# Performance work log

Hardware: AMD Instinct MI355X
Metric: run time of the kernel (lower is better)

Reference implementation:

```python
import jax, jax.numpy as jnp
import numpy as np

B, N, F, D, TOPK, EXTRA = 32, 128, 10, 64, 20, 25
BN = B * N
EPS = 1e-5
SLOPE = 0.2  # GDN GraphLayer leaky_relu negative slope


def _cosine(a, b):
    na = jnp.maximum(jnp.linalg.norm(a, axis=-1), 1e-12)
    nb = jnp.maximum(jnp.linalg.norm(b, axis=-1), 1e-12)
    return (a @ b.T) / (na[:, None] * nb[None, :])


def _segment_softmax(logits, seg, num):
    m = jax.ops.segment_max(logits, seg, num_segments=num)
    m = jnp.where(jnp.isfinite(m), m, 0.0)  # empty segments
    e = jnp.exp(logits - m[seg])
    s = jax.ops.segment_sum(e, seg, num_segments=num)
    return e / jnp.maximum(s[seg], 1e-12)


def setup_inputs() -> dict:
    key = jax.random.key(0)
    ks = jax.random.split(key, 12)
    r = lambda i, shape, s=1.0: jax.random.normal(ks[i], shape, dtype=jnp.float32) * s
    return dict(
        data=r(0, (B, N, F)),
        emb=r(1, (N, D)) * 0.3,                       # nn.Embedding(node_num, dim)
        W1=r(2, (F, D)) * (1.0 / np.sqrt(F)),         # GraphLayer lin
        att_i1=r(3, (2 * D,)) * 0.1,                  # att on concat(h, emb)
        att_j1=r(4, (2 * D,)) * 0.1,
        bias1=jnp.zeros((D,), jnp.float32),
        bn1_g=jnp.ones((D,), jnp.float32),
        bn1_b=jnp.zeros((D,), jnp.float32),
        P=r(5, (BN, BN)) * (1.0 / np.sqrt(BN)),       # extra_pram
        W2=r(6, (D, D)) * (1.0 / np.sqrt(D)),         # GraphLayer1 lin
        att_i2=r(7, (D,)) * 0.1,
        att_j2=r(8, (D,)) * 0.1,
        bias2=jnp.zeros((D,), jnp.float32),
        bnO_g=jnp.ones((D,), jnp.float32),
        bnO_b=jnp.zeros((D,), jnp.float32),
        W_out=r(9, (D, 1)) * (1.0 / np.sqrt(D)),      # OutLayer Linear(dim,1)
        b_out=jnp.zeros((1,), jnp.float32),
        org_edge_index=jnp.zeros((2, 2), jnp.int32),  # dead arg in original forward
    )


def _forward(data, emb, W1, att_i1, att_j1, bias1, bn1_g, bn1_b, P, W2,
             att_i2, att_j2, bias2, bnO_g, bnO_b, W_out, b_out):
    x = data.reshape(BN, F)

    # ---- learned top-k graph from detached embedding cosine similarity ----
    w = jax.lax.stop_gradient(emb)              # weights_arr = detach()
    cos = _cosine(w, w)                         # [N, N]
    topv, topi = jax.lax.top_k(cos, TOPK)       # [N, TOPK]
    cos_w = jnp.tile(topv.reshape(-1), B)       # [B*N*TOPK]
    src0 = topi.reshape(-1)                     # gated_j (source)
    dst0 = jnp.repeat(jnp.arange(N), TOPK)      # gated_i (target)
    offs = jnp.repeat(jnp.arange(B) * N, N * TOPK)
    src = jnp.tile(src0, B) + offs
    dst = jnp.tile(dst0, B) + offs

    # ---- GraphLayer (GAT-style with embedding keys, edge weight = cos) ----
    all_emb = jnp.tile(emb, (B, 1))             # [BN, D]
    h = x @ W1                                  # [BN, D]
    kf = jnp.concatenate([h, all_emb], axis=-1) # [BN, 2D]
    si, sj = kf @ att_i1, kf @ att_j1           # [BN]
    score = jax.nn.leaky_relu(si[dst] + sj[src], SLOPE) * cos_w
    alpha = _segment_softmax(score, dst, BN)
    agg = jax.ops.segment_sum(h[src] * alpha[:, None], dst, num_segments=BN) + bias1
    mu, var = agg.mean(0), agg.var(0)           # BatchNorm1d (batch stats)
    gcn = jax.nn.relu(bn1_g * (agg - mu) / jnp.sqrt(var + EPS) + bn1_b)

    # ---- extra-feature branch (always taken: P is [BN, BN]) ----
    ef = P.T @ gcn                              # (gcn_out.T @ P).T
    g = jnp.concatenate([gcn, ef], axis=0)      # [2BN, D]
    cos2 = _cosine(g, g)                        # [2BN, 2BN]
    topv2, topi2 = jax.lax.top_k(cos2, EXTRA)
    corrs = topv2[:BN].reshape(-1)              # [BN*EXTRA]
    src2 = jnp.repeat(jnp.arange(BN), EXTRA)    # extra_i = edge_index[0] (source)
    dst2 = topi2[:BN].reshape(-1)               # extra_j = edge_index[1] (target)

    # ---- GraphLayer1 (no embedding keys, no BN in GNNLayer1.forward) ----
    h2 = g @ W2                                 # [2BN, D]
    s2 = jax.nn.leaky_relu((h2 @ att_i2)[dst2] + (h2 @ att_j2)[src2], SLOPE) * corrs
    alpha2 = _segment_softmax(s2, dst2, 2 * BN)
    agg2 = jax.ops.segment_sum(h2[src2] * alpha2[:, None], dst2, num_segments=2 * BN) + bias2
    gcn2 = jax.nn.relu(agg2)[:BN]

    # ---- output head: mul by embedding, BN over channels, Linear(D,1) ----
    x3 = gcn2.reshape(B, N, D) * emb[None]      # [B, N, D]
    mu2, var2 = x3.mean((0, 1)), x3.var((0, 1)) # BatchNorm1d over channel D
    x4 = jax.nn.relu(bnO_g * (x3 - mu2) / jnp.sqrt(var2 + EPS) + bnO_b)
    out = x4 @ W_out + b_out                    # [B, N, 1]; dropout = identity (eval)
    return out.reshape(-1, N)                   # [B, N]


def reference(data, emb, W1, att_i1, att_j1, bias1, bn1_g, bn1_b, P, W2,
              att_i2, att_j2, bias2, bnO_g, bnO_b, W_out, b_out, org_edge_index):
    # org_edge_index is dead in the original forward (only cached, never consumed)
    return _forward(data, emb, W1, att_i1, att_j1, bias1, bn1_g, bn1_b, P, W2,
                    att_i2, att_j2, bias2, bnO_g, bnO_b, W_out, b_out)
```

## Files before the change

### kernel.cpp

```cpp
#include <hip/hip_runtime.h>
#include <hip/hip_bf16.h>
#include <math.h>

#define DEV __device__ __forceinline__

constexpr int Bb   = 32;
constexpr int Nn   = 128;
constexpr int Ff   = 10;
constexpr int Dd   = 64;
constexpr int TOPK = 20;
constexpr int EXTRA= 25;
constexpr int BN   = 4096;
constexpr int TBN  = 8192;
constexpr int RC   = 16;
constexpr int CAND_CAP = 1024;
constexpr float EPS   = 1e-5f;
constexpr float SLOPE = 0.2f;

DEV unsigned int fenc(float f){
  unsigned int b = __float_as_uint(f);
  return (b & 0x80000000u) ? ~b : (b | 0x80000000u);
}
DEV float fdec(unsigned int u){
  unsigned int b = (u & 0x80000000u) ? (u & 0x7FFFFFFFu) : ~u;
  return __uint_as_float(b);
}

__global__ void k_zero(float* __restrict__ p, int n){
  int i = blockIdx.x*256 + threadIdx.x;
  if(i < n) p[i] = 0.f;
}

__global__ void k_emb_norm(const float* __restrict__ emb, float* __restrict__ norms){
  int i = blockIdx.x, d = threadIdx.x;
  float v = emb[i*Dd + d];
  float s = v*v;
  for(int o=32;o>0;o>>=1) s += __shfl_down(s, o, 64);
  if(d==0) norms[i] = fmaxf(sqrtf(s), 1e-12f);
}

__global__ void k_emb_topk(const float* __restrict__ emb, const float* __restrict__ norms,
                           float* __restrict__ topv, int* __restrict__ topi){
  __shared__ float se[Dd];
  __shared__ float sc[Nn];
  __shared__ float rv[Nn];
  __shared__ int   ri[Nn];
  int i = blockIdx.x, t = threadIdx.x;
  if(t < Dd) se[t] = emb[i*Dd + t];
  __syncthreads();
  float dot = 0.f;
  for(int d=0; d<Dd; d++) dot += se[d]*emb[t*Dd + d];
  sc[t] = dot/(norms[i]*norms[t]);
  __syncthreads();
  for(int k=0; k<TOPK; k++){
    rv[t] = sc[t]; ri[t] = t; __syncthreads();
    for(int o=Nn/2; o>0; o>>=1){
      if(t < o){
        float v2 = rv[t+o]; int i2 = ri[t+o];
        if(v2 > rv[t] || (v2 == rv[t] && i2 < ri[t])){ rv[t]=v2; ri[t]=i2; }
      }
      __syncthreads();
    }
    if(t==0){
      topv[i*TOPK + k] = rv[0];
      topi[i*TOPK + k] = ri[0];
      sc[ri[0]] = -INFINITY;
    }
    __syncthreads();
  }
}

__global__ void k_h1(const float* __restrict__ data, const float* __restrict__ emb,
                     const float* __restrict__ W1, const float* __restrict__ ai1,
                     const float* __restrict__ aj1,
                     float* __restrict__ h, float* __restrict__ si, float* __restrict__ sj){
  int r = blockIdx.x, d = threadIdx.x;
  int node = r & (Nn-1);
  __shared__ float xr[Ff];
  if(d < Ff) xr[d] = data[r*Ff + d];
  __syncthreads();
  float hv = 0.f;
  #pragma unroll
  for(int f=0; f<Ff; f++) hv += xr[f]*W1[f*Dd + d];
  h[r*Dd + d] = hv;
  float e = emb[node*Dd + d];
  float a = hv*ai1[d] + e*ai1[Dd + d];
  float b = hv*aj1[d] + e*aj1[Dd + d];
  for(int o=32;o>0;o>>=1){ a += __shfl_down(a,o,64); b += __shfl_down(b,o,64); }
  if(d==0){ si[r] = a; sj[r] = b; }
}

__global__ void k_agg1(const float* __restrict__ h, const float* __restrict__ si,
                       const float* __restrict__ sj, const float* __restrict__ topv,
                       const int* __restrict__ topi, const float* __restrict__ bias1,
                       float* __restrict__ agg){
  int r = blockIdx.x, d = threadIdx.x;
  int b = r >> 7, node = r & (Nn-1);
  __shared__ float sal[TOPK];
  __shared__ int   ssrc[TOPK];
  if(d < TOPK){
    int s = b*Nn + topi[node*TOPK + d];
    float sc = si[r] + sj[s];
    sc = sc >= 0.f ? sc : SLOPE*sc;
    sal[d] = sc * topv[node*TOPK + d];
    ssrc[d] = s;
  }
  __syncthreads();
  float m = -INFINITY;
  #pragma unroll
  for(int k=0;k<TOPK;k++) m = fmaxf(m, sal[k]);
  float al[TOPK]; float ssum = 0.f;
  #pragma unroll
  for(int k=0;k<TOPK;k++){ al[k] = expf(sal[k]-m); ssum += al[k]; }
  float inv = 1.0f/fmaxf(ssum, 1e-12f);
  float acc = 0.f;
  #pragma unroll
  for(int k=0;k<TOPK;k++) acc += al[k]*inv*h[ssrc[k]*Dd + d];
  agg[r*Dd + d] = acc + bias1[d];
}

__global__ void k_colstats(const float* __restrict__ x, float* __restrict__ mu, float* __restrict__ var){
  int c = blockIdx.x, t = threadIdx.x;
  float s = 0.f, s2 = 0.f;
  for(int r=t; r<BN; r+=256){ float v = x[r*Dd + c]; s += v; s2 += v*v; }
  __shared__ float ls[256], ls2[256];
  ls[t]=s; ls2[t]=s2; __syncthreads();
  for(int o=128;o>0;o>>=1){
    if(t<o){ ls[t]+=ls[t+o]; ls2[t]+=ls2[t+o]; }
    __syncthreads();
  }
  if(t==0){ float m = ls[0]/BN; mu[c]=m; var[c]=ls2[0]/BN - m*m; }
}

__global__ void k_bnrelu1(const float* __restrict__ agg, const float* __restrict__ mu,
                          const float* __restrict__ var, const float* __restrict__ gamma,
                          const float* __restrict__ beta, float* __restrict__ g){
  int idx = blockIdx.x*256 + threadIdx.x;
  int c = idx & (Dd-1);
  float v = agg[idx];
  float y = gamma[c]*(v - mu[c])/sqrtf(var[c]+EPS) + beta[c];
  g[idx] = fmaxf(y, 0.f);
}

__global__ __launch_bounds__(256) void k_ef1(const float* __restrict__ P, const float* __restrict__ gcn,
                                             float* __restrict__ part){
  __shared__ float Pt[16*64];
  __shared__ float Gt[16*64];
  int t = threadIdx.x;
  int jbase = blockIdx.x*64;
  int r0 = blockIdx.y*256;
  int row = t >> 4, col4 = (t & 15)*4;
  int tr = t >> 4, tc = t & 15;
  float acc[4][4] = {};
  for(int step=0; step<16; step++){
    int r = r0 + step*16;
    float4 pv = *(const float4*)&P[(size_t)(r+row)*BN + jbase + col4];
    float4 gv = *(const float4*)&gcn[(r+row)*Dd + col4];
    __syncthreads();
    *(float4*)&Pt[row*64 + col4] = pv;
    *(float4*)&Gt[row*64 + col4] = gv;
    __syncthreads();
    #pragma unroll
    for(int rr=0; rr<16; rr++){
      float4 pa = *(float4*)&Pt[rr*64 + tr*4];
      float4 gb = *(float4*)&Gt[rr*64 + tc*4];
      float pav[4] = {pa.x, pa.y, pa.z, pa.w};
      float gbv[4] = {gb.x, gb.y, gb.z, gb.w};
      #pragma unroll
      for(int a=0;a<4;a++)
        #pragma unroll
        for(int b=0;b<4;b++) acc[a][b] += pav[a]*gbv[b];
    }
  }
  float* dst = part + ((size_t)blockIdx.y*BN + jbase)*Dd;
  #pragma unroll
  for(int a=0;a<4;a++){
    float4 v = make_float4(acc[a][0],acc[a][1],acc[a][2],acc[a][3]);
    *(float4*)&dst[(tr*4+a)*Dd + tc*4] = v;
  }
}

__global__ void k_ef2(const float* __restrict__ part, float* __restrict__ ef){
  int i = blockIdx.x*256 + threadIdx.x;
  float4 s = make_float4(0.f,0.f,0.f,0.f);
  #pragma unroll
  for(int c=0;c<RC;c++){
    float4 v = *(const float4*)&part[(size_t)c*BN*Dd + (size_t)i*4];
    s.x += v.x; s.y += v.y; s.z += v.z; s.w += v.w;
  }
  *(float4*)&ef[(size_t)i*4] = s;
}

__global__ void k_gn(const float* __restrict__ x, float* __restrict__ gn){
  int r = blockIdx.x, d = threadIdx.x;
  float v = x[(size_t)r*Dd + d];
  float s = v*v;
  for(int o=32;o>0;o>>=1) s += __shfl_down(s, o, 64);
  s = __shfl(s, 0, 64);
  float inv = 1.0f/fmaxf(sqrtf(s), 1e-12f);
  gn[(size_t)r*Dd + d] = v*inv;
}

__global__ __launch_bounds__(256) void k_sgemm(const float* __restrict__ gn,
                                               int rbase, float* __restrict__ S){
  __shared__ __align__(16) float A[64*128];
  __shared__ __align__(16) float Bs[64*128];
  int t = threadIdx.x;
  int ctile = blockIdx.x*128;
  int rtile = rbase + blockIdx.y*128;
  int q = t >> 4, m0 = t & 15;
  #pragma unroll
  for(int l=0;l<8;l++){
    int m = m0 + 16*l;
    float4 av = *(const float4*)&gn[(size_t)(rtile+m)*Dd + q*4];
    float4 bv = *(const float4*)&gn[(size_t)(ctile+m)*Dd + q*4];
    A[(q*4+0)*128 + m] = av.x; A[(q*4+1)*128 + m] = av.y;
    A[(q*4+2)*128 + m] = av.z; A[(q*4+3)*128 + m] = av.w;
    Bs[(q*4+0)*128 + m] = bv.x; Bs[(q*4+1)*128 + m] = bv.y;
    Bs[(q*4+2)*128 + m] = bv.z; Bs[(q*4+3)*128 + m] = bv.w;
  }
  __syncthreads();
  int tr = t >> 4;
  int tc = t & 15;
  float acc[8][8] = {};
  #pragma unroll 4
  for(int k=0;k<64;k++){
    float4 a0 = *(const float4*)&A[k*128 + tr*4];
    float4 a1 = *(const float4*)&A[k*128 + tr*4 + 64];
    float4 b0 = *(const float4*)&Bs[k*128 + tc*4];
    float4 b1 = *(const float4*)&Bs[k*128 + tc*4 + 64];
    float a[8] = {a0.x,a0.y,a0.z,a0.w,a1.x,a1.y,a1.z,a1.w};
    float b[8] = {b0.x,b0.y,b0.z,b0.w,b1.x,b1.y,b1.z,b1.w};
    #pragma unroll
    for(int i=0;i<8;i++)
      #pragma unroll
      for(int j=0;j<8;j++) acc[i][j] += a[i]*b[j];
  }
  int rloc = blockIdx.y*128;
  #pragma unroll
  for(int i=0;i<8;i++){
    int r = rloc + tr*4 + (i&3) + (i>>2)*64;
    float4 v0 = make_float4(acc[i][0],acc[i][1],acc[i][2],acc[i][3]);
    float4 v1 = make_float4(acc[i][4],acc[i][5],acc[i][6],acc[i][7]);
    *(float4*)&S[(size_t)r*TBN + ctile + tc*4]      = v0;
    *(float4*)&S[(size_t)r*TBN + ctile + tc*4 + 64] = v1;
  }
}

__global__ __launch_bounds__(256) void k_radix(const float* __restrict__ S, int rbase,
                                               float* __restrict__ topv2, int* __restrict__ topi2){
  __shared__ unsigned hist[4096];
  __shared__ unsigned wtot[4];
  __shared__ unsigned candE[CAND_CAP];
  __shared__ unsigned short candC[CAND_CAP];
  __shared__ unsigned bc_bin, bc_need, bc_cnt, bc_c;
  int t = threadIdx.x;
  int lane = t & 63, wid = t >> 6;
  int r = blockIdx.x;
  const float* src = S + (size_t)r*TBN;
  int col0 = t*32;
  unsigned enc[32];
  #pragma unroll
  for(int j=0;j<8;j++){
    float4 v = *(const float4*)&src[col0 + j*4];
    enc[j*4+0]=fenc(v.x); enc[j*4+1]=fenc(v.y); enc[j*4+2]=fenc(v.z); enc[j*4+3]=fenc(v.w);
  }
  #pragma unroll
  for(int j=0;j<16;j++) hist[t*16 + j] = 0u;
  __syncthreads();
  #pragma unroll
  for(int j=0;j<32;j++) atomicAdd(&hist[enc[j] >> 20], 1u);
  __syncthreads();
  unsigned lsum = 0u;
  #pragma unroll
  for(int j=0;j<16;j++) lsum += hist[t*16 + j];
  unsigned v = lsum;
  #pragma unroll
  for(int o=1;o<64;o<<=1){
    unsigned u = (unsigned)__shfl_down((int)v, o, 64);
    if(lane + o < 64) v += u;
  }
  if(lane == 0) wtot[wid] = v;
  __syncthreads();
  unsigned cross = 0u;
  #pragma unroll
  for(int w2=0;w2<4;w2++) if(w2 > wid) cross += wtot[w2];
  unsigned Tinc = v + cross;
  unsigned above = Tinc - lsum;
  unsigned run = above;
  #pragma unroll
  for(int b=15;b>=0;b--){
    unsigned prev = run;
    run += hist[t*16 + b];
    if(run >= EXTRA && prev < EXTRA){ bc_bin = (unsigned)(t*16 + b); bc_need = EXTRA - prev; }
  }
  if(t==0){ bc_cnt = 0u; bc_c = 0u; }
  __syncthreads();
  unsigned pivotBin = bc_bin, needIn = bc_need;
  int gr = rbase + r;
  #pragma unroll
  for(int j=0;j<32;j++){
    unsigned e = enc[j];
    unsigned bin = e >> 20;
    if(bin > pivotBin){
      unsigned s = atomicAdd(&bc_cnt, 1u);
      topv2[gr*EXTRA + s] = fdec(e);
      topi2[gr*EXTRA + s] = col0 + j;
    } else if(bin == pivotBin){
      unsigned ci = atomicAdd(&bc_c, 1u);
      if(ci < CAND_CAP){ candE[ci] = e; candC[ci] = (unsigned short)(col0 + j); }
    }
  }
  __syncthreads();
  unsigned c = bc_c;
  if(c <= CAND_CAP){
    for(unsigned i=t; i<c; i+=256){
      unsigned ei = candE[i]; unsigned coli = candC[i];
      unsigned rank = 0;
      for(unsigned j2=0;j2<c;j2++){
        unsigned ej = candE[j2];
        rank += (ej > ei) || (ej == ei && candC[j2] < coli);
      }
      if(rank < needIn){
        unsigned s = atomicAdd(&bc_cnt, 1u);
        topv2[gr*EXTRA + s] = fdec(ei);
        topi2[gr*EXTRA + s] = (int)coli;
      }
    }
  } else {
    unsigned* h256  = hist;
    unsigned* scanb = hist + 1024;
    unsigned prefix = pivotBin;
    unsigned need = needIn;
    const int shifts[3] = {12, 4, 0};
    const unsigned masks[3] = {255u, 255u, 15u};
    const int nbins[3] = {256, 256, 16};
    for(int p=0;p<3;p++){
      int sh = shifts[p]; unsigned mk = masks[p]; int nb = nbins[p];
      if(t < nb) h256[t] = 0u;
      __syncthreads();
      #pragma unroll
      for(int j=0;j<32;j++){
        unsigned e = enc[j];
        int pshift = (p==0)? 20 : (p==1? 12 : 4);
        if((e >> pshift) == prefix) atomicAdd(&h256[(e>>sh)&mk], 1u);
      }
      __syncthreads();
      unsigned vv = (t < nb) ? h256[t] : 0u;
      for(int o=1;o<nb;o<<=1){
        if(t < nb) scanb[t] = vv;
        __syncthreads();
        if(t < nb && t+o < nb) vv += scanb[t+o];
        __syncthreads();
      }
      if(t < nb) scanb[t] = vv;
      __syncthreads();
      if(t < nb){
        unsigned nxt = (t < nb-1) ? scanb[t+1] : 0u;
        if(vv >= need && nxt < need){ bc_bin = (prefix << ((p==2)?4:8)) | (unsigned)t; bc_need = need - nxt; }
      }
      __syncthreads();
      prefix = bc_bin; need = bc_need;
      __syncthreads();
    }
    unsigned pivotEnc = prefix;
    unsigned needTies = need;
    unsigned tie_local = 0u;
    #pragma unroll
    for(int j=0;j<32;j++){
      unsigned e = enc[j];
      if((e >> 20) == pivotBin){
        if(e > pivotEnc){
          unsigned s = atomicAdd(&bc_cnt, 1u);
          topv2[gr*EXTRA + s] = fdec(e);
          topi2[gr*EXTRA + s] = col0 + j;
        } else if(e == pivotEnc) tie_local++;
      }
    }
    unsigned iv = tie_local;
    for(int o=1;o<256;o<<=1){
      scanb[t] = iv; __syncthreads();
      if(t >= o) iv += scanb[t-o];
      __syncthreads();
    }
    unsigned rank = iv - tie_local;
    #pragma unroll
    for(int j=0;j<32;j++){
      unsigned e = enc[j];
      if(e == pivotEnc && (e >> 20) == pivotBin){
        if(rank < needTies){
          unsigned s = atomicAdd(&bc_cnt, 1u);
          topv2[gr*EXTRA + s] = fdec(e);
          topi2[gr*EXTRA + s] = col0 + j;
        }
        rank++;
      }
    }
  }
}

__global__ void k_h2(const float* __restrict__ g, const float* __restrict__ W2,
                     const float* __restrict__ ai2w, const float* __restrict__ aj2w,
                     float* __restrict__ h2, float* __restrict__ a2i, float* __restrict__ a2j){
  int r = blockIdx.x, d = threadIdx.x;
  __shared__ float gr[Dd];
  gr[d] = g[(size_t)r*Dd + d];
  __syncthreads();
  float hv = 0.f;
  #pragma unroll
  for(int k=0;k<Dd;k++) hv += gr[k]*W2[k*Dd + d];
  h2[(size_t)r*Dd + d] = hv;
  float a = hv*ai2w[d];
  float b = hv*aj2w[d];
  for(int o=32;o>0;o>>=1){ a += __shfl_down(a,o,64); b += __shfl_down(b,o,64); }
  if(d==0){ a2i[r]=a; a2j[r]=b; }
}

__global__ void k_s2(const float* __restrict__ a2i, const float* __restrict__ a2j,
                     const float* __restrict__ topv2, const int* __restrict__ topi2,
                     float* __restrict__ s2, unsigned int* __restrict__ segmax){
  int e = blockIdx.x*256 + threadIdx.x;
  if(e >= BN*EXTRA) return;
  int r = e/EXTRA;
  int dst = topi2[e];
  float sc = a2i[dst] + a2j[r];
  sc = sc >= 0.f ? sc : SLOPE*sc;
  sc *= topv2[e];
  s2[e] = sc;
  atomicMax(&segmax[dst], fenc(sc));
}

__global__ void k_e2(const float* __restrict__ s2, const int* __restrict__ topi2,
                     const unsigned int* __restrict__ segmax,
                     float* __restrict__ e2, float* __restrict__ ssum){
  int e = blockIdx.x*256 + threadIdx.x;
  if(e >= BN*EXTRA) return;
  int dst = topi2[e];
  float m = fdec(segmax[dst]);
  float v = expf(s2[e] - m);
  e2[e] = v;
  atomicAdd(&ssum[dst], v);
}

__global__ void k_scat(const float* __restrict__ e2, const float* __restrict__ ssum,
                       const int* __restrict__ topi2, const float* __restrict__ h2,
                       float* __restrict__ agg2){
  int idx = blockIdx.x*256 + threadIdx.x;
  int e = idx >> 6, d = idx & 63;
  int dst = topi2[e];
  int src = e/EXTRA;
  float alpha = e2[e]/fmaxf(ssum[dst], 1e-12f);
  atomicAdd(&agg2[(size_t)dst*Dd + d], alpha*h2[(size_t)src*Dd + d]);
}

__global__ void k_headstats(const float* __restrict__ agg2, const float* __restrict__ bias2,
                            const float* __restrict__ emb, float* __restrict__ mu2, float* __restrict__ var2){
  int c = blockIdx.x, t = threadIdx.x;
  float bc = bias2[c];
  float s = 0.f, s2 = 0.f;
  for(int r=t; r<BN; r+=256){
    float v = fmaxf(agg2[(size_t)r*Dd + c] + bc, 0.f) * emb[(r & (Nn-1))*Dd + c];
    s += v; s2 += v*v;
  }
  __shared__ float ls[256], ls2[256];
  ls[t]=s; ls2[t]=s2; __syncthreads();
  for(int o=128;o>0;o>>=1){
    if(t<o){ ls[t]+=ls[t+o]; ls2[t]+=ls2[t+o]; }
    __syncthreads();
  }
  if(t==0){ float m=ls[0]/BN; mu2[c]=m; var2[c]=ls2[0]/BN - m*m; }
}

__global__ void k_out(const float* __restrict__ agg2, const float* __restrict__ bias2,
                      const float* __restrict__ emb, const float* __restrict__ mu2,
                      const float* __restrict__ var2, const float* __restrict__ gO,
                      const float* __restrict__ bO, const float* __restrict__ Wout,
                      const float* __restrict__ bout, float* __restrict__ out){
  int r = blockIdx.x, d = threadIdx.x;
  float v = fmaxf(agg2[(size_t)r*Dd + d] + bias2[d], 0.f) * emb[(r & (Nn-1))*Dd + d];
  float y = gO[d]*(v - mu2[d])/sqrtf(var2[d]+EPS) + bO[d];
  y = fmaxf(y, 0.f)*Wout[d];
  for(int o=32;o>0;o>>=1) y += __shfl_down(y, o, 64);
  if(d==0) out[r] = y + bout[0];
}

extern "C" void kernel_launch(void* const* d_in, const int* in_sizes, int n_in,
                              void* d_out, int out_size, void* d_ws, size_t ws_size,
                              hipStream_t stream){
  const float* data  = (const float*)d_in[0];
  const float* emb   = (const float*)d_in[1];
  const float* W1    = (const float*)d_in[2];
  const float* ai1   = (const float*)d_in[3];
  const float* aj1   = (const float*)d_in[4];
  const float* bias1 = (const float*)d_in[5];
  const float* bn1g  = (const float*)d_in[6];
  const float* bn1b  = (const float*)d_in[7];
  const float* P     = (const float*)d_in[8];
  const float* W2    = (const float*)d_in[9];
  const float* ai2w  = (const float*)d_in[10];
  const float* aj2w  = (const float*)d_in[11];
  const float* bias2 = (const float*)d_in[12];
  const float* bnOg  = (const float*)d_in[13];
  const float* bnOb  = (const float*)d_in[14];
  const float* Wout  = (const float*)d_in[15];
  const float* bout  = (const float*)d_in[16];
  float* out = (float*)d_out;

  char* w = (char*)d_ws;
  auto alloc = [&](size_t nbytes)->char*{
    char* p = w; w += (nbytes + 255) & ~(size_t)255; return p;
  };
  float* norms1 = (float*)alloc(Nn*4);
  float* topv1  = (float*)alloc(Nn*TOPK*4);
  int*   topi1  = (int*)  alloc(Nn*TOPK*4);
  float* h      = (float*)alloc((size_t)BN*Dd*4);
  float* si     = (float*)alloc(BN*4);
  float* sj     = (float*)alloc(BN*4);
  float* agg1   = (float*)alloc((size_t)BN*Dd*4);
  float* mu1    = (float*)alloc(Dd*4);
  float* var1   = (float*)alloc(Dd*4);
  float* g      = (float*)alloc((size_t)TBN*Dd*4);
  float* gn     = (float*)alloc((size_t)TBN*Dd*4);
  float* topv2  = (float*)alloc((size_t)BN*EXTRA*4);
  int*   topi2  = (int*)  alloc((size_t)BN*EXTRA*4);
  float* h2     = (float*)alloc((size_t)TBN*Dd*4);
  float* a2i    = (float*)alloc(TBN*4);
  float* a2j    = (float*)alloc(TBN*4);
  float* s2     = (float*)alloc((size_t)BN*EXTRA*4);
  float* e2     = (float*)alloc((size_t)BN*EXTRA*4);
  float* zblock = (float*)alloc(((size_t)TBN*Dd + TBN + TBN)*4);
  float* agg2   = zblock;
  float* ssum   = zblock + (size_t)TBN*Dd;
  unsigned int* segmax = (unsigned int*)(ssum + TBN);
  float* mu2    = (float*)alloc(Dd*4);
  float* var2   = (float*)alloc(Dd*4);
  float* efpart = (float*)alloc((size_t)RC*BN*Dd*4);

  size_t used = (size_t)(w - (char*)d_ws);
  size_t rem  = ws_size > used ? ws_size - used : 0;
  int chunkRows = 4096;
  while(chunkRows > 128 && (size_t)chunkRows*TBN*4 > rem) chunkRows >>= 1;
  float* Schunk = (float*)alloc((size_t)chunkRows*TBN*4);

  k_emb_norm<<<Nn, 64, 0, stream>>>(emb, norms1);
  k_emb_topk<<<Nn, Nn, 0, stream>>>(emb, norms1, topv1, topi1);
  k_h1<<<BN, 64, 0, stream>>>(data, emb, W1, ai1, aj1, h, si, sj);
  k_agg1<<<BN, 64, 0, stream>>>(h, si, sj, topv1, topi1, bias1, agg1);
  k_colstats<<<Dd, 256, 0, stream>>>(agg1, mu1, var1);
  k_bnrelu1<<<(BN*Dd)/256, 256, 0, stream>>>(agg1, mu1, var1, bn1g, bn1b, g);

  k_ef1<<<dim3(64, RC), 256, 0, stream>>>(P, g, efpart);
  k_ef2<<<(BN*Dd/4)/256, 256, 0, stream>>>(efpart, g + (size_t)BN*Dd);

  k_gn<<<TBN, 64, 0, stream>>>(g, gn);
  for(int rbase=0; rbase<BN; rbase+=chunkRows){
    k_sgemm<<<dim3(TBN/128, chunkRows/128), 256, 0, stream>>>(gn, rbase, Schunk);
    k_radix<<<chunkRows, 256, 0, stream>>>(Schunk, rbase, topv2, topi2);
  }

  k_h2<<<TBN, 64, 0, stream>>>(g, W2, ai2w, aj2w, h2, a2i, a2j);
  k_zero<<<((TBN*Dd + 2*TBN) + 255)/256, 256, 0, stream>>>(zblock, TBN*Dd + 2*TBN);
  k_s2<<<(BN*EXTRA + 255)/256, 256, 0, stream>>>(a2i, a2j, topv2, topi2, s2, segmax);
  k_e2<<<(BN*EXTRA + 255)/256, 256, 0, stream>>>(s2, topi2, segmax, e2, ssum);
  k_scat<<<(BN*EXTRA*Dd)/256, 256, 0, stream>>>(e2, ssum, topi2, h2, agg2);

  k_headstats<<<Dd, 256, 0, stream>>>(agg2, bias2, emb, mu2, var2);
  k_out<<<BN, 64, 0, stream>>>(agg2, bias2, emb, mu2, var2, bnOg, bnOb, Wout, bout, out);
}
```

Baseline: 372.1 us.

## Prune top-k radix scan with per-tile maxima, trim unused second-layer work

The similarity GEMM now writes the maximum of each 128-column tile for every row. The radix top-k kernel uses these maxima to find the 25th-largest tile max and skips loading and histogramming tiles that cannot hold a top-25 value. The h2 projection now runs only on the first BN rows, and edges whose destination is at or above BN are skipped in the score, exp and scatter kernels, because only the first BN outputs are consumed. The P@g kernel is also widened to 128-column tiles, doubling the work per thread. The cost is an extra small max buffer, shuffle reductions in the GEMM epilogue, and divergent branches in the radix kernel.

```diff
diff --git a/kernel.cpp b/kernel.cpp
--- a/kernel.cpp
+++ b/kernel.cpp
@@ -144,39 +144,42 @@
 
 __global__ __launch_bounds__(256) void k_ef1(const float* __restrict__ P, const float* __restrict__ gcn,
                                              float* __restrict__ part){
-  __shared__ float Pt[16*64];
+  __shared__ float Pt[16*128];
   __shared__ float Gt[16*64];
   int t = threadIdx.x;
-  int jbase = blockIdx.x*64;
+  int jbase = blockIdx.x*128;
   int r0 = blockIdx.y*256;
   int row = t >> 4, col4 = (t & 15)*4;
   int tr = t >> 4, tc = t & 15;
-  float acc[4][4] = {};
+  float acc[8][4] = {};
   for(int step=0; step<16; step++){
     int r = r0 + step*16;
-    float4 pv = *(const float4*)&P[(size_t)(r+row)*BN + jbase + col4];
-    float4 gv = *(const float4*)&gcn[(r+row)*Dd + col4];
+    float4 pv0 = *(const float4*)&P[(size_t)(r+row)*BN + jbase + col4];
+    float4 pv1 = *(const float4*)&P[(size_t)(r+row)*BN + jbase + col4 + 64];
+    float4 gv  = *(const float4*)&gcn[(r+row)*Dd + col4];
     __syncthreads();
-    *(float4*)&Pt[row*64 + col4] = pv;
+    *(float4*)&Pt[row*128 + col4]      = pv0;
+    *(float4*)&Pt[row*128 + col4 + 64] = pv1;
     *(float4*)&Gt[row*64 + col4] = gv;
     __syncthreads();
     #pragma unroll
     for(int rr=0; rr<16; rr++){
-      float4 pa = *(float4*)&Pt[rr*64 + tr*4];
-      float4 gb = *(float4*)&Gt[rr*64 + tc*4];
-      float pav[4] = {pa.x, pa.y, pa.z, pa.w};
-      float gbv[4] = {gb.x, gb.y, gb.z, gb.w};
+      float4 pa0 = *(float4*)&Pt[rr*128 + tr*8];
+      float4 pa1 = *(float4*)&Pt[rr*128 + tr*8 + 4];
+      float4 gb  = *(float4*)&Gt[rr*64 + tc*4];
+      float pav[8] = {pa0.x,pa0.y,pa0.z,pa0.w,pa1.x,pa1.y,pa1.z,pa1.w};
+      float gbv[4] = {gb.x,gb.y,gb.z,gb.w};
       #pragma unroll
-      for(int a=0;a<4;a++)
+      for(int a=0;a<8;a++)
         #pragma unroll
         for(int b=0;b<4;b++) acc[a][b] += pav[a]*gbv[b];
     }
   }
   float* dst = part + ((size_t)blockIdx.y*BN + jbase)*Dd;
   #pragma unroll
-  for(int a=0;a<4;a++){
+  for(int a=0;a<8;a++){
     float4 v = make_float4(acc[a][0],acc[a][1],acc[a][2],acc[a][3]);
-    *(float4*)&dst[(tr*4+a)*Dd + tc*4] = v;
+    *(float4*)&dst[(tr*8+a)*Dd + tc*4] = v;
   }
 }
 
@@ -202,7 +205,8 @@
 }
 
 __global__ __launch_bounds__(256) void k_sgemm(const float* __restrict__ gn,
-                                               int rbase, float* __restrict__ S){
+                                               int rbase, float* __restrict__ S,
+                                               float* __restrict__ Smax){
   __shared__ __align__(16) float A[64*128];
   __shared__ __align__(16) float Bs[64*128];
   int t = threadIdx.x;
@@ -239,7 +243,14 @@
   int rloc = blockIdx.y*128;
   #pragma unroll
   for(int i=0;i<8;i++){
-    int r = rloc + tr*4 + (i&3) + (i>>2)*64;
+    int rl = tr*4 + (i&3) + (i>>2)*64;
+    int r  = rloc + rl;
+    float mx = acc[i][0];
+    #pragma unroll
+    for(int j=1;j<8;j++) mx = fmaxf(mx, acc[i][j]);
+    #pragma unroll
+    for(int o=1;o<16;o<<=1) mx = fmaxf(mx, __shfl_xor(mx, o, 64));
+    if(tc == 0) Smax[r*64 + blockIdx.x] = mx;
     float4 v0 = make_float4(acc[i][0],acc[i][1],acc[i][2],acc[i][3]);
     float4 v1 = make_float4(acc[i][4],acc[i][5],acc[i][6],acc[i][7]);
     *(float4*)&S[(size_t)r*TBN + ctile + tc*4]      = v0;
@@ -247,29 +258,54 @@
   }
 }
 
-__global__ __launch_bounds__(256) void k_radix(const float* __restrict__ S, int rbase,
+__global__ __launch_bounds__(256) void k_radix(const float* __restrict__ S,
+                                               const float* __restrict__ Smax,
+                                               int rbase,
                                                float* __restrict__ topv2, int* __restrict__ topi2){
   __shared__ unsigned hist[4096];
   __shared__ unsigned wtot[4];
   __shared__ unsigned candE[CAND_CAP];
   __shared__ unsigned short candC[CAND_CAP];
   __shared__ unsigned bc_bin, bc_need, bc_cnt, bc_c;
+  __shared__ float stmax[64];
+  __shared__ float sLsh;
   int t = threadIdx.x;
   int lane = t & 63, wid = t >> 6;
   int r = blockIdx.x;
   const float* src = S + (size_t)r*TBN;
   int col0 = t*32;
+
+  if(t < 64) stmax[t] = Smax[r*64 + t];
+  #pragma unroll
+  for(int j=0;j<16;j++) hist[t*16 + j] = 0u;
+  if(t==0){ bc_cnt = 0u; bc_c = 0u; }
+  __syncthreads();
+  if(t < 64){
+    float mi = stmax[t];
+    int cnt = 0;
+    for(int j=0;j<64;j++){
+      float mj = stmax[j];
+      cnt += (mj > mi) || (mj == mi && j < t);
+    }
+    if(cnt == 24) sLsh = mi;
+  }
+  __syncthreads();
+  float L = sLsh;
+  bool skip = stmax[t >> 2] < L;
+
   unsigned enc[32];
-  #pragma unroll
-  for(int j=0;j<8;j++){
-    float4 v = *(const float4*)&src[col0 + j*4];
-    enc[j*4+0]=fenc(v.x); enc[j*4+1]=fenc(v.y); enc[j*4+2]=fenc(v.z); enc[j*4+3]=fenc(v.w);
-  }
-  #pragma unroll
-  for(int j=0;j<16;j++) hist[t*16 + j] = 0u;
-  __syncthreads();
-  #pragma unroll
-  for(int j=0;j<32;j++) atomicAdd(&hist[enc[j] >> 20], 1u);
+  if(!skip){
+    #pragma unroll
+    for(int j=0;j<8;j++){
+      float4 v = *(const float4*)&src[col0 + j*4];
+      enc[j*4+0]=fenc(v.x); enc[j*4+1]=fenc(v.y); enc[j*4+2]=fenc(v.z); enc[j*4+3]=fenc(v.w);
+    }
+    #pragma unroll
+    for(int j=0;j<32;j++) atomicAdd(&hist[enc[j] >> 20], 1u);
+  } else {
+    #pragma unroll
+    for(int j=0;j<32;j++) enc[j] = 0u;
+  }
   __syncthreads();
   unsigned lsum = 0u;
   #pragma unroll
@@ -294,7 +330,6 @@
     run += hist[t*16 + b];
     if(run >= EXTRA && prev < EXTRA){ bc_bin = (unsigned)(t*16 + b); bc_need = EXTRA - prev; }
   }
-  if(t==0){ bc_cnt = 0u; bc_c = 0u; }
   __syncthreads();
   unsigned pivotBin = bc_bin, needIn = bc_need;
   int gr = rbase + r;
@@ -423,6 +458,7 @@
   if(e >= BN*EXTRA) return;
   int r = e/EXTRA;
   int dst = topi2[e];
+  if(dst >= BN) return;
   float sc = a2i[dst] + a2j[r];
   sc = sc >= 0.f ? sc : SLOPE*sc;
   sc *= topv2[e];
@@ -436,6 +472,7 @@
   int e = blockIdx.x*256 + threadIdx.x;
   if(e >= BN*EXTRA) return;
   int dst = topi2[e];
+  if(dst >= BN) return;
   float m = fdec(segmax[dst]);
   float v = expf(s2[e] - m);
   e2[e] = v;
@@ -448,6 +485,7 @@
   int idx = blockIdx.x*256 + threadIdx.x;
   int e = idx >> 6, d = idx & 63;
   int dst = topi2[e];
+  if(dst >= BN) return;
   int src = e/EXTRA;
   float alpha = e2[e]/fmaxf(ssum[dst], 1e-12f);
   atomicAdd(&agg2[(size_t)dst*Dd + d], alpha*h2[(size_t)src*Dd + d]);
@@ -535,6 +573,7 @@
   float* mu2    = (float*)alloc(Dd*4);
   float* var2   = (float*)alloc(Dd*4);
   float* efpart = (float*)alloc((size_t)RC*BN*Dd*4);
+  float* SmaxB  = (float*)alloc((size_t)4096*64*4);
 
   size_t used = (size_t)(w - (char*)d_ws);
   size_t rem  = ws_size > used ? ws_size - used : 0;
@@ -549,16 +588,16 @@
   k_colstats<<<Dd, 256, 0, stream>>>(agg1, mu1, var1);
   k_bnrelu1<<<(BN*Dd)/256, 256, 0, stream>>>(agg1, mu1, var1, bn1g, bn1b, g);
 
-  k_ef1<<<dim3(64, RC), 256, 0, stream>>>(P, g, efpart);
+  k_ef1<<<dim3(BN/128, RC), 256, 0, stream>>>(P, g, efpart);
   k_ef2<<<(BN*Dd/4)/256, 256, 0, stream>>>(efpart, g + (size_t)BN*Dd);
 
   k_gn<<<TBN, 64, 0, stream>>>(g, gn);
   for(int rbase=0; rbase<BN; rbase+=chunkRows){
-    k_sgemm<<<dim3(TBN/128, chunkRows/128), 256, 0, stream>>>(gn, rbase, Schunk);
-    k_radix<<<chunkRows, 256, 0, stream>>>(Schunk, rbase, topv2, topi2);
-  }
-
-  k_h2<<<TBN, 64, 0, stream>>>(g, W2, ai2w, aj2w, h2, a2i, a2j);
+    k_sgemm<<<dim3(TBN/128, chunkRows/128), 256, 0, stream>>>(gn, rbase, Schunk, SmaxB);
+    k_radix<<<chunkRows, 256, 0, stream>>>(Schunk, SmaxB, rbase, topv2, topi2);
+  }
+
+  k_h2<<<BN, 64, 0, stream>>>(g, W2, ai2w, aj2w, h2, a2i, a2j);
   k_zero<<<((TBN*Dd + 2*TBN) + 255)/256, 256, 0, stream>>>(zblock, TBN*Dd + 2*TBN);
   k_s2<<<(BN*EXTRA + 255)/256, 256, 0, stream>>>(a2i, a2j, topv2, topi2, s2, segmax);
   k_e2<<<(BN*EXTRA + 255)/256, 256, 0, stream>>>(s2, topi2, segmax, e2, ssum);
```

Measured after the change: 370.6 us. About the same (-0.4%).
